# Performance work log

Measured on AMD Instinct MI355X. Metric: run time of the kernel, lower is better.

The kernel has to match this reference:

```python
import jax, jax.numpy as jnp
import numpy as np

H, HS, C = 16, 64, 1024  # num_heads, head_size, n_embd

def setup_inputs() -> dict:
    key = jax.random.key(0)
    ks = jax.random.split(key, 5)
    B, T = 2, 2048
    s = 1.0 / np.sqrt(C)
    return {
        "x": jax.random.normal(ks[0], (B, T, C), dtype=jnp.float32),
        "Wq": jax.random.normal(ks[1], (H, C, HS), dtype=jnp.float32) * s,
        "Wk": jax.random.normal(ks[2], (H, C, HS), dtype=jnp.float32) * s,
        "Wv": jax.random.normal(ks[3], (H, C, HS), dtype=jnp.float32) * s,
        "Wo": jax.random.normal(ks[4], (C, C), dtype=jnp.float32) * s,
    }

def reference(x, Wq, Wk, Wv, Wo):
    B, T, Cdim = x.shape
    scale = Cdim ** -0.5  # original scales by n_embd**-0.5, not head_size
    q = jnp.einsum('btc,hcd->bhtd', x, Wq)
    k = jnp.einsum('btc,hcd->bhtd', x, Wk)
    v = jnp.einsum('btc,hcd->bhtd', x, Wv)
    wei = jnp.einsum('bhtd,bhsd->bhts', q, k) * scale  # [B,H,T,T]
    causal = jnp.tril(jnp.ones((T, T), dtype=bool))
    wei = jnp.where(causal, wei, -jnp.inf)
    wei = jax.nn.softmax(wei, axis=-1)
    out = jnp.einsum('bhts,bhsd->bhtd', wei, v)  # [B,H,T,HS]
    out = out.transpose(0, 2, 1, 3).reshape(B, T, -1)  # concat heads -> [B,T,C]
    return out @ Wo.T
```

## Files before the change

### kernel.cpp

```cpp
#include <hip/hip_runtime.h>

typedef unsigned short ushort_t;
typedef __bf16 bf16x8 __attribute__((ext_vector_type(8)));
typedef float f32x4 __attribute__((ext_vector_type(4)));
typedef float f32x16 __attribute__((ext_vector_type(16)));
typedef unsigned short ushortx8 __attribute__((ext_vector_type(8)));
typedef unsigned int uintx4 __attribute__((ext_vector_type(4)));

#define NH 16
#define HS 64
#define CD 1024
#define NB 2
#define NT 2048
#define BT (NB * NT)
#define N3 (3 * CD)

#define L2E_DIV32 0.04508422002778011f

#define QKV_LD 2048
#define SLOT_BYTES 18432
#define WAVE_BYTES 4608
#define R0_SLOTS 796

__constant__ static const int QB_TAB[32] = {
  10,10,15,15, 4, 9, 9,13,14,14,14,15, 8, 8,12,12,
  13,13, 3, 7, 7,11,11,11,12, 6, 6, 2, 5, 5, 1, 0};
__constant__ static const int T0_TAB[32] = {
   0,11, 0,11, 0, 0,10, 0, 0,10,20,22, 0, 9, 0, 9,
  10,19, 0, 0, 8, 0, 8,16,18, 0, 7, 0, 0, 6, 0, 0};
__constant__ static const int T1_TAB[32] = {
  11,22,11,22,10,10,20,10,10,20,30,32, 9,18, 9,18,
  19,28, 8, 8,16, 8,16,24,26, 7,14, 6, 6,12, 4, 2};
__constant__ static const int K_TAB[32] = {
   2, 2, 3, 3, 1, 2, 2, 3, 3, 3, 3, 3, 2, 2, 3, 3,
   3, 3, 1, 2, 2, 3, 3, 3, 3, 2, 2, 1, 2, 2, 1, 1};
__constant__ static const int MC_TAB[11][3] = {
  {28,29, 0}, {25,26, 0}, {19,20, 0}, {12,13, 0}, { 5, 6, 0}, { 0, 1, 0},
  {21,22,23}, {14,15,24}, { 7,16,17}, { 8, 9,10}, { 2, 3,11}};


__device__ __forceinline__ ushort_t bf16_rne(float f) {
  union { float f; unsigned u; } v; v.f = f;
  unsigned u = v.u;
  unsigned r = (u + 0x7FFFu + ((u >> 16) & 1u)) >> 16;
  return (ushort_t)r;
}

__device__ __forceinline__ float bf2f(ushort_t u) {
  union { unsigned u; float f; } v; v.u = ((unsigned)u) << 16; return v.f;
}

__device__ __forceinline__ void gload_lds16(const ushort_t* g, ushort_t* l) {
  __builtin_amdgcn_global_load_lds(
      (const __attribute__((address_space(1))) unsigned int*)g,
      (__attribute__((address_space(3))) unsigned int*)l, 16, 0, 0);
}

__device__ __forceinline__ f32x4 mfma16(ushortx8 a, ushortx8 b, f32x4 c) {
  return __builtin_amdgcn_mfma_f32_16x16x32_bf16(
      __builtin_bit_cast(bf16x8, a), __builtin_bit_cast(bf16x8, b), c, 0, 0, 0);
}

__device__ __forceinline__ f32x16 mfma32(ushortx8 a, ushortx8 b, f32x16 c) {
  return __builtin_amdgcn_mfma_f32_32x32x16_bf16(
      __builtin_bit_cast(bf16x8, a), __builtin_bit_cast(bf16x8, b), c, 0, 0, 0);
}

__device__ __forceinline__ unsigned cvt_pk_bf16(float lo, float hi) {
  unsigned r;
  asm("v_cvt_pk_bf16_f32 %0, %1, %2" : "=v"(r) : "v"(lo), "v"(hi));
  return r;
}

__device__ __forceinline__ void plswap(unsigned &a, unsigned &b) {
  asm volatile("v_permlane32_swap_b32 %0, %1" : "+v"(a), "+v"(b));
}

__device__ __forceinline__ const char* slot_ptr(const char* wsb, const char* dout, int s) {
  return (s < R0_SLOTS) ? wsb + (size_t)s * SLOT_BYTES
                        : dout + (size_t)(s - R0_SLOTS) * SLOT_BYTES;
}


__global__ __launch_bounds__(256)
void pack_cast2(const float4* __restrict__ x, ushort_t* __restrict__ xout,
                const float4* __restrict__ wo, ushort_t* __restrict__ woout) {
  const int bid = blockIdx.x;
  const float4* in = (bid < 4096) ? x : wo;
  ushort_t* out = (bid < 4096) ? xout : woout;
  const int i = ((bid < 4096) ? bid : (bid - 4096)) * 256 + threadIdx.x;
  const float4 v = in[i];
  ushort4 r;
  r.x = bf16_rne(v.x); r.y = bf16_rne(v.y);
  r.z = bf16_rne(v.z); r.w = bf16_rne(v.w);
  *(ushort4*)(out + (size_t)i * 4) = r;
}

__global__ __launch_bounds__(256)
void pack_wqkv(const float* __restrict__ Wq, const float* __restrict__ Wk,
               const float* __restrict__ Wv, ushort_t* __restrict__ out) {
  __shared__ ushort_t tile[64 * 66];
  const int sh = blockIdx.y;
  const int s = sh >> 4, h = sh & 15;
  const float* W = (s == 0) ? Wq : ((s == 1) ? Wk : Wv);
  const int c0 = blockIdx.x * 64;
  const int t = threadIdx.x;
#pragma unroll
  for (int j = 0; j < 16; ++j) {
    const int idx = t + j * 256;
    const int ci = idx >> 6, d = idx & 63;
    const float v = W[(size_t)(h * 1024 + c0 + ci) * 64 + d];
    tile[d * 66 + ci] = bf16_rne(v);
  }
  __syncthreads();
#pragma unroll
  for (int j = 0; j < 16; ++j) {
    const int idx = t + j * 256;
    const int d = idx >> 6, ci = idx & 63;
    out[(size_t)(s * 1024 + h * 64 + d) * 1024 + c0 + ci] = tile[d * 66 + ci];
  }
}


template <int MODE>
__global__ __launch_bounds__(256)
void gemm_bt(const ushort_t* __restrict__ A, const ushort_t* __restrict__ Bt,
             void* __restrict__ Cv, ushort_t* __restrict__ Vt,
             int M, int N, int K) {
  __shared__ __align__(16) ushort_t ldsA[2][128 * 32];
  __shared__ __align__(16) ushort_t ldsB[2][128 * 32];
  const int tid = threadIdx.x;
  const int lane = tid & 63;
  const int wave = tid >> 6;
  const int row0 = blockIdx.y * 128;
  const int col0 = blockIdx.x * 128;
  const int wm = wave >> 1, wn = wave & 1;

  f32x4 acc[4][4] = {};

  const int ce = (tid & 3) * 8;

  auto stage = [&](int buf, int kt) {
    const int kbase = kt * 32;
#pragma unroll
    for (int j = 0; j < 2; ++j) {
      const int r = j * 64 + (tid >> 2);
      gload_lds16(A + (size_t)(row0 + r) * K + kbase + ce,
                  &ldsA[buf][(j * 256 + wave * 64) * 8]);
      gload_lds16(Bt + (size_t)(col0 + r) * K + kbase + ce,
                  &ldsB[buf][(j * 256 + wave * 64) * 8]);
    }
  };

  const int arow_off = (wm * 64 + (lane & 15)) * 32 + (lane >> 4) * 8;
  const int brow_off = (wn * 64 + (lane & 15)) * 32 + (lane >> 4) * 8;

  auto compute = [&](int buf) {
    ushortx8 af[4], bfr[4];
#pragma unroll
    for (int m = 0; m < 4; ++m)
      af[m] = *(const ushortx8*)&ldsA[buf][arow_off + m * 512];
#pragma unroll
    for (int n = 0; n < 4; ++n)
      bfr[n] = *(const ushortx8*)&ldsB[buf][brow_off + n * 512];
#pragma unroll
    for (int m = 0; m < 4; ++m)
#pragma unroll
      for (int n = 0; n < 4; ++n)
        acc[m][n] = mfma16(af[m], bfr[n], acc[m][n]);
  };

  stage(0, 0);
  __syncthreads();
  const int nk = K >> 5;
  for (int kt = 0; kt < nk; ++kt) {
    const int cur = kt & 1;
    if (kt + 1 < nk) stage(cur ^ 1, kt + 1);
    compute(cur);
    __syncthreads();
  }

#pragma unroll
  for (int m = 0; m < 4; ++m) {
    const int rbase = row0 + wm * 64 + m * 16 + (lane >> 4) * 4;
#pragma unroll
    for (int n = 0; n < 4; ++n) {
      const int col = col0 + wn * 64 + n * 16 + (lane & 15);
      if constexpr (MODE == 0) {
#pragma unroll
        for (int i = 0; i < 4; ++i)
          ((float*)Cv)[(size_t)(rbase + i) * N + col] = acc[m][n][i];
      } else {
        if (col < 2048) {
          const float sc = (col < 1024) ? L2E_DIV32 : 1.0f;
#pragma unroll
          for (int i = 0; i < 4; ++i)
            ((ushort_t*)Cv)[(size_t)(rbase + i) * QKV_LD + col] =
                bf16_rne(acc[m][n][i] * sc);
        } else {
          const int dcol = col - 2048;
          const int bI = rbase >> 11;
          const int t0i = rbase & 2047;
          ushort4 pk;
          pk.x = bf16_rne(acc[m][n][0]);
          pk.y = bf16_rne(acc[m][n][1]);
          pk.z = bf16_rne(acc[m][n][2]);
          pk.w = bf16_rne(acc[m][n][3]);
          *(ushort4*)(Vt + (size_t)(bI * 1024 + dcol) * NT + t0i) = pk;
        }
      }
    }
  }
}


__global__ __launch_bounds__(256, 4)
void attn_fwd11(const ushort_t* __restrict__ QKV, const ushort_t* __restrict__ Vt,
                ushort_t* __restrict__ O, char* __restrict__ wsb,
                char* __restrict__ dout) {
  __shared__ __align__(16) ushort_t KV[2][2][4096];

  const int tid = threadIdx.x;
  const int lane = tid & 63;
  const int w = tid >> 6;
  const int l31 = lane & 31;
  const int h = lane >> 5;

  const int x = blockIdx.x;
  const int bh = x & 31;
  const int c = x >> 5;
  const int qb = QB_TAB[c];
  const int k  = K_TAB[c];
  const int t0 = T0_TAB[c];
  const int t1 = T1_TAB[c];
  const int nt = 2 * qb + 2;
  const bool lastc = (t1 == nt);

  const int b = bh >> 4, head = bh & 15;
  const size_t base = (size_t)b * NT * QKV_LD;
  const int qg = qb * 128 + w * 32 + l31;
  const int tmax = lastc ? (2 * qb + (w >> 1)) : (t1 - 1);

  int koff[4];
#pragma unroll
  for (int kc = 0; kc < 4; ++kc)
    koff[kc] = l31 * 128 + (((2 * kc + h) ^ (l31 & 7)) * 16);

  const int rowA = tid >> 3, ccA = tid & 7;
  const int rowB = 32 + rowA;
  const ushort_t* kg = QKV + base + 1024 + head * 64;
  const ushort_t* vg = Vt + (size_t)(bh * 64) * NT;
  const ushort_t* ksA = kg + (size_t)(t0 * 64 + rowA) * QKV_LD + ((ccA ^ (rowA & 7)) * 8);
  const ushort_t* ksB = kg + (size_t)(t0 * 64 + rowB) * QKV_LD + ((ccA ^ (rowB & 7)) * 8);
  const ushort_t* vsA = vg + (size_t)rowA * NT + t0 * 64 + ((ccA ^ (rowA & 7)) * 8);
  const ushort_t* vsB = vg + (size_t)rowB * NT + t0 * 64 + ((ccA ^ (rowB & 7)) * 8);
  const size_t kadv = (size_t)64 * QKV_LD;

  gload_lds16(ksA, &KV[0][0][w * 512]);
  gload_lds16(ksB, &KV[0][0][2048 + w * 512]);
  gload_lds16(vsA, &KV[0][1][w * 512]);
  gload_lds16(vsB, &KV[0][1][2048 + w * 512]);

  ushortx8 qf[4];
  {
    const ushort_t* qp = QKV + base + (size_t)qg * QKV_LD + head * 64 + h * 8;
#pragma unroll
    for (int kc = 0; kc < 4; ++kc) qf[kc] = *(const ushortx8*)(qp + kc * 16);
  }

  f32x16 oA = {}, oB = {};
  float m_r = -INFINITY, l_r = 0.f;

  auto half_pass = [&](f32x16 s, const char* vb, const int kc0, const bool msk) {
    if (msk) {
#pragma unroll
      for (int r = 0; r < 16; ++r) {
        const int krow = (r & 3) + 8 * (r >> 2) + 4 * h;
        if (krow > l31) s[r] = -INFINITY;
      }
    }
    float mm[8];
#pragma unroll
    for (int r = 0; r < 8; ++r) mm[r] = fmaxf(s[r], s[r + 8]);
#pragma unroll
    for (int st = 4; st >= 1; st >>= 1)
#pragma unroll
      for (int r = 0; r < st; ++r) mm[r] = fmaxf(mm[r], mm[r + st]);
    const float mx = fmaxf(mm[0], __shfl_xor(mm[0], 32, 64));
    if (__any(mx > m_r + 8.0f)) {
      const float mn = fmaxf(m_r, mx);
      const float al = exp2f(m_r - mn);
      m_r = mn; l_r *= al;
#pragma unroll
      for (int r = 0; r < 16; ++r) { oA[r] *= al; oB[r] *= al; }
    }
    unsigned u[8];
    float ps[4];
#pragma unroll
    for (int jj = 0; jj < 4; ++jj) ps[jj] = 0.f;
#pragma unroll
    for (int jj = 0; jj < 8; ++jj) {
      const float e0 = exp2f(s[2 * jj] - m_r);
      const float e1 = exp2f(s[2 * jj + 1] - m_r);
      u[jj] = cvt_pk_bf16(e0, e1);
      ps[jj & 3] += e0 + e1;
    }
    ps[0] += ps[2]; ps[1] += ps[3]; ps[0] += ps[1];
    l_r += ps[0] + __shfl_xor(ps[0], 32, 64);
    plswap(u[0], u[2]); plswap(u[1], u[3]);
    plswap(u[4], u[6]); plswap(u[5], u[7]);
#pragma unroll
    for (int q2 = 0; q2 < 2; ++q2) {
      uintx4 pw;
      pw[0] = u[4 * q2 + 0]; pw[1] = u[4 * q2 + 1];
      pw[2] = u[4 * q2 + 2]; pw[3] = u[4 * q2 + 3];
      const ushortx8 pav = __builtin_bit_cast(ushortx8, pw);
      oA = mfma32(*(const ushortx8*)(vb + koff[kc0 + q2]), pav, oA);
      oB = mfma32(*(const ushortx8*)(vb + 4096 + koff[kc0 + q2]), pav, oB);
    }
  };

  int curb = 0;
  for (int t = t0; t < t1; ++t) {
    const int nxt = curb ^ 1;
    if (t + 1 < t1) {
      ksA += kadv; ksB += kadv; vsA += 64; vsB += 64;
      gload_lds16(ksA, &KV[nxt][0][w * 512]);
      gload_lds16(ksB, &KV[nxt][0][2048 + w * 512]);
      gload_lds16(vsA, &KV[nxt][1][w * 512]);
      gload_lds16(vsB, &KV[nxt][1][2048 + w * 512]);
      asm volatile("s_waitcnt vmcnt(4)" ::: "memory");
    } else {
      asm volatile("s_waitcnt vmcnt(0)" ::: "memory");
    }
    __builtin_amdgcn_s_barrier();
    asm volatile("" ::: "memory");

    if (t <= tmax) {
      const bool diag = lastc && (t == tmax);
      const bool halfB = diag && ((w & 1) == 0);
      const char* kb = (const char*)&KV[curb][0][0];
      const char* vb = (const char*)&KV[curb][1][0];

      {
        f32x16 sA = {};
#pragma unroll
        for (int kc = 0; kc < 4; ++kc)
          sA = mfma32(*(const ushortx8*)(kb + koff[kc]), qf[kc], sA);
        half_pass(sA, vb, 0, diag && halfB);
      }
      if (!halfB) {
        f32x16 sB = {};
#pragma unroll
        for (int kc = 0; kc < 4; ++kc)
          sB = mfma32(*(const ushortx8*)(kb + 4096 + koff[kc]), qf[kc], sB);
        half_pass(sB, vb, 2, diag);
      }
    }

    __builtin_amdgcn_s_barrier();
    asm volatile("" ::: "memory");
    curb ^= 1;
  }

  if (k == 1) {
    const float inv_l = 1.0f / l_r;
    ushort_t* op = O + ((size_t)(b * NT + qg)) * 1024 + head * 64;
#pragma unroll
    for (int db = 0; db < 2; ++db)
#pragma unroll
      for (int g = 0; g < 4; ++g) {
        ushort4 pk;
        pk.x = bf16_rne((db ? oB[4 * g + 0] : oA[4 * g + 0]) * inv_l);
        pk.y = bf16_rne((db ? oB[4 * g + 1] : oA[4 * g + 1]) * inv_l);
        pk.z = bf16_rne((db ? oB[4 * g + 2] : oA[4 * g + 2]) * inv_l);
        pk.w = bf16_rne((db ? oB[4 * g + 3] : oA[4 * g + 3]) * inv_l);
        *(ushort4*)(op + db * 32 + 8 * g + 4 * h) = pk;
      }
  } else {
    const int s = bh * 32 + c;
    char* wb = (char*)slot_ptr(wsb, dout, s) + w * WAVE_BYTES;
#pragma unroll
    for (int g = 0; g < 4; ++g) {
      ushortx8 pk;
#pragma unroll
      for (int e2 = 0; e2 < 8; ++e2)
        pk[e2] = bf16_rne(g < 2 ? oA[g * 8 + e2] : oB[(g - 2) * 8 + e2]);
      *(ushortx8*)(wb + lane * 64 + g * 16) = pk;
    }
    *(float*)(wb + 4096 + lane * 4) = m_r;
    *(float*)(wb + 4352 + lane * 4) = l_r;
  }
}

__global__ __launch_bounds__(256)
void attn_merge(const char* __restrict__ wsb, const char* __restrict__ dout,
                ushort_t* __restrict__ O) {
  const int x = blockIdx.x;
  const int bh = x & 31;
  const int qi = x >> 5;
  const int qb = 5 + qi;
  const int k = (qb <= 10) ? 2 : 3;
  const int tid = threadIdx.x;
  const int lane = tid & 63;
  const int w = tid >> 6;
  const int l31 = lane & 31;
  const int h = lane >> 5;

  float M = -INFINITY;
  for (int jj = 0; jj < k; ++jj) {
    const int s = bh * 32 + MC_TAB[qi][jj];
    const char* wb = slot_ptr(wsb, dout, s) + w * WAVE_BYTES;
    M = fmaxf(M, *(const float*)(wb + 4096 + lane * 4));
  }
  float o[32];
#pragma unroll
  for (int r = 0; r < 32; ++r) o[r] = 0.f;
  float lacc = 0.f;
  for (int jj = 0; jj < k; ++jj) {
    const int s = bh * 32 + MC_TAB[qi][jj];
    const char* wb = slot_ptr(wsb, dout, s) + w * WAVE_BYTES;
    const float a = exp2f(*(const float*)(wb + 4096 + lane * 4) - M);
    lacc += a * *(const float*)(wb + 4352 + lane * 4);
#pragma unroll
    for (int g = 0; g < 4; ++g) {
      const ushortx8 v = *(const ushortx8*)(wb + lane * 64 + g * 16);
#pragma unroll
      for (int e = 0; e < 8; ++e) o[g * 8 + e] += a * bf2f(v[e]);
    }
  }
  const float inv_l = 1.0f / lacc;
  const int b = bh >> 4, head = bh & 15;
  const int qg = qb * 128 + w * 32 + l31;
  ushort_t* op = O + ((size_t)(b * NT + qg)) * 1024 + head * 64;
#pragma unroll
  for (int db = 0; db < 2; ++db)
#pragma unroll
    for (int g = 0; g < 4; ++g) {
      ushort4 pk;
      pk.x = bf16_rne(o[db * 16 + 4 * g + 0] * inv_l);
      pk.y = bf16_rne(o[db * 16 + 4 * g + 1] * inv_l);
      pk.z = bf16_rne(o[db * 16 + 4 * g + 2] * inv_l);
      pk.w = bf16_rne(o[db * 16 + 4 * g + 3] * inv_l);
      *(ushort4*)(op + db * 32 + 8 * g + 4 * h) = pk;
    }
}


extern "C" void kernel_launch(void* const* d_in, const int* in_sizes, int n_in,
                              void* d_out, int out_size, void* d_ws, size_t ws_size,
                              hipStream_t stream) {
  (void)in_sizes; (void)n_in; (void)out_size; (void)ws_size;
  const float* x  = (const float*)d_in[0];
  const float* Wq = (const float*)d_in[1];
  const float* Wk = (const float*)d_in[2];
  const float* Wv = (const float*)d_in[3];
  const float* Wo = (const float*)d_in[4];

  char* ws = (char*)d_ws;
  ushort_t* Xbf    = (ushort_t*)(ws);
  ushort_t* Wqkv_t = (ushort_t*)(ws + 8388608);
  ushort_t* Wo_bf  = (ushort_t*)(ws + 14680064);
  ushort_t* QKV    = (ushort_t*)(ws + 16777216);
  ushort_t* Vt     = (ushort_t*)(ws + 33554432);
  ushort_t* Obf    = (ushort_t*)(ws + 41943040);

  pack_cast2<<<5120, 256, 0, stream>>>((const float4*)x, Xbf, (const float4*)Wo, Wo_bf);
  pack_wqkv<<<dim3(16, 48), 256, 0, stream>>>(Wq, Wk, Wv, Wqkv_t);

  gemm_bt<1><<<dim3(24, 32), 256, 0, stream>>>(Xbf, Wqkv_t, QKV, Vt, BT, N3, CD);
  attn_fwd11<<<1024, 256, 0, stream>>>(QKV, Vt, Obf, ws, (char*)d_out);
  attn_merge<<<352, 256, 0, stream>>>(ws, (char*)d_out, Obf);
  gemm_bt<0><<<dim3(8, 32), 256, 0, stream>>>(Obf, Wo_bf, d_out, nullptr, BT, CD, CD);
}
```

Baseline: 122.8 us.

## Split GEMM kernels, use 128x64 tiles for output projection, add MFMA priority hints

Splits the templated GEMM into a dedicated QKV kernel and a new 128x64-tile GEMM for the output projection. The new tile doubles the grid from 256 to 512 blocks so the CUs stay busier. The attention kernel now raises wave priority around its MFMA sequences with s_setprio and uses a flatter 3-way max tree for the row max. The smaller tile brings lower per-block reuse and more redundant A loads.

```diff
diff --git a/kernel.cpp b/kernel.cpp
--- a/kernel.cpp
+++ b/kernel.cpp
@@ -122,11 +122,9 @@
 }
 
 
-template <int MODE>
 __global__ __launch_bounds__(256)
-void gemm_bt(const ushort_t* __restrict__ A, const ushort_t* __restrict__ Bt,
-             void* __restrict__ Cv, ushort_t* __restrict__ Vt,
-             int M, int N, int K) {
+void gemm_bt_qkv(const ushort_t* __restrict__ A, const ushort_t* __restrict__ Bt,
+                 ushort_t* __restrict__ QKVo, ushort_t* __restrict__ Vt, int K) {
   __shared__ __align__(16) ushort_t ldsA[2][128 * 32];
   __shared__ __align__(16) ushort_t ldsB[2][128 * 32];
   const int tid = threadIdx.x;
@@ -186,36 +184,99 @@
 #pragma unroll
     for (int n = 0; n < 4; ++n) {
       const int col = col0 + wn * 64 + n * 16 + (lane & 15);
-      if constexpr (MODE == 0) {
+      if (col < 2048) {
+        const float sc = (col < 1024) ? L2E_DIV32 : 1.0f;
 #pragma unroll
         for (int i = 0; i < 4; ++i)
-          ((float*)Cv)[(size_t)(rbase + i) * N + col] = acc[m][n][i];
+          QKVo[(size_t)(rbase + i) * QKV_LD + col] = bf16_rne(acc[m][n][i] * sc);
       } else {
-        if (col < 2048) {
-          const float sc = (col < 1024) ? L2E_DIV32 : 1.0f;
-#pragma unroll
-          for (int i = 0; i < 4; ++i)
-            ((ushort_t*)Cv)[(size_t)(rbase + i) * QKV_LD + col] =
-                bf16_rne(acc[m][n][i] * sc);
-        } else {
-          const int dcol = col - 2048;
-          const int bI = rbase >> 11;
-          const int t0i = rbase & 2047;
-          ushort4 pk;
-          pk.x = bf16_rne(acc[m][n][0]);
-          pk.y = bf16_rne(acc[m][n][1]);
-          pk.z = bf16_rne(acc[m][n][2]);
-          pk.w = bf16_rne(acc[m][n][3]);
-          *(ushort4*)(Vt + (size_t)(bI * 1024 + dcol) * NT + t0i) = pk;
-        }
+        const int dcol = col - 2048;
+        const int bI = rbase >> 11;
+        const int t0i = rbase & 2047;
+        ushort4 pk;
+        pk.x = bf16_rne(acc[m][n][0]);
+        pk.y = bf16_rne(acc[m][n][1]);
+        pk.z = bf16_rne(acc[m][n][2]);
+        pk.w = bf16_rne(acc[m][n][3]);
+        *(ushort4*)(Vt + (size_t)(bI * 1024 + dcol) * NT + t0i) = pk;
       }
     }
   }
 }
 
 
+__global__ __launch_bounds__(256)
+void gemm_bt64(const ushort_t* __restrict__ A, const ushort_t* __restrict__ Bt,
+               float* __restrict__ C, int M, int N, int K) {
+  __shared__ __align__(16) ushort_t ldsA[2][128 * 32];
+  __shared__ __align__(16) ushort_t ldsB[2][64 * 32];
+  const int tid = threadIdx.x;
+  const int lane = tid & 63;
+  const int wave = tid >> 6;
+  const int row0 = blockIdx.y * 128;
+  const int col0 = blockIdx.x * 64;
+  const int wm = wave >> 1, wn = wave & 1;
+
+  f32x4 acc[4][2] = {};
+
+  const int ce = (tid & 3) * 8;
+
+  auto stage = [&](int buf, int kt) {
+    const int kbase = kt * 32;
+#pragma unroll
+    for (int j = 0; j < 2; ++j) {
+      const int r = j * 64 + (tid >> 2);
+      gload_lds16(A + (size_t)(row0 + r) * K + kbase + ce,
+                  &ldsA[buf][(j * 256 + wave * 64) * 8]);
+    }
+    gload_lds16(Bt + (size_t)(col0 + (tid >> 2)) * K + kbase + ce,
+                &ldsB[buf][(wave * 64) * 8]);
+  };
+
+  const int arow_off = (wm * 64 + (lane & 15)) * 32 + (lane >> 4) * 8;
+  const int brow_off = (wn * 32 + (lane & 15)) * 32 + (lane >> 4) * 8;
+
+  auto compute = [&](int buf) {
+    ushortx8 af[4], bfr[2];
+#pragma unroll
+    for (int m = 0; m < 4; ++m)
+      af[m] = *(const ushortx8*)&ldsA[buf][arow_off + m * 512];
+#pragma unroll
+    for (int n = 0; n < 2; ++n)
+      bfr[n] = *(const ushortx8*)&ldsB[buf][brow_off + n * 512];
+#pragma unroll
+    for (int m = 0; m < 4; ++m)
+#pragma unroll
+      for (int n = 0; n < 2; ++n)
+        acc[m][n] = mfma16(af[m], bfr[n], acc[m][n]);
+  };
+
+  stage(0, 0);
+  __syncthreads();
+  const int nk = K >> 5;
+  for (int kt = 0; kt < nk; ++kt) {
+    const int cur = kt & 1;
+    if (kt + 1 < nk) stage(cur ^ 1, kt + 1);
+    compute(cur);
+    __syncthreads();
+  }
+
+#pragma unroll
+  for (int m = 0; m < 4; ++m) {
+    const int rbase = row0 + wm * 64 + m * 16 + (lane >> 4) * 4;
+#pragma unroll
+    for (int n = 0; n < 2; ++n) {
+      const int col = col0 + wn * 32 + n * 16 + (lane & 15);
+#pragma unroll
+      for (int i = 0; i < 4; ++i)
+        C[(size_t)(rbase + i) * N + col] = acc[m][n][i];
+    }
+  }
+}
+
+
 __global__ __launch_bounds__(256, 4)
-void attn_fwd11(const ushort_t* __restrict__ QKV, const ushort_t* __restrict__ Vt,
+void attn_fwd13(const ushort_t* __restrict__ QKV, const ushort_t* __restrict__ Vt,
                 ushort_t* __restrict__ O, char* __restrict__ wsb,
                 char* __restrict__ dout) {
   __shared__ __align__(16) ushort_t KV[2][2][4096];
@@ -279,14 +340,15 @@
         if (krow > l31) s[r] = -INFINITY;
       }
     }
-    float mm[8];
-#pragma unroll
-    for (int r = 0; r < 8; ++r) mm[r] = fmaxf(s[r], s[r + 8]);
-#pragma unroll
-    for (int st = 4; st >= 1; st >>= 1)
-#pragma unroll
-      for (int r = 0; r < st; ++r) mm[r] = fmaxf(mm[r], mm[r + st]);
-    const float mx = fmaxf(mm[0], __shfl_xor(mm[0], 32, 64));
+    const float t0m = fmaxf(fmaxf(s[0], s[1]), s[2]);
+    const float t1m = fmaxf(fmaxf(s[3], s[4]), s[5]);
+    const float t2m = fmaxf(fmaxf(s[6], s[7]), s[8]);
+    const float t3m = fmaxf(fmaxf(s[9], s[10]), s[11]);
+    const float t4m = fmaxf(fmaxf(s[12], s[13]), s[14]);
+    const float u0m = fmaxf(fmaxf(t0m, t1m), t2m);
+    const float u1m = fmaxf(fmaxf(t3m, t4m), s[15]);
+    float mx = fmaxf(u0m, u1m);
+    mx = fmaxf(mx, __shfl_xor(mx, 32, 64));
     if (__any(mx > m_r + 8.0f)) {
       const float mn = fmaxf(m_r, mx);
       const float al = exp2f(m_r - mn);
@@ -309,6 +371,7 @@
     l_r += ps[0] + __shfl_xor(ps[0], 32, 64);
     plswap(u[0], u[2]); plswap(u[1], u[3]);
     plswap(u[4], u[6]); plswap(u[5], u[7]);
+    __builtin_amdgcn_s_setprio(1);
 #pragma unroll
     for (int q2 = 0; q2 < 2; ++q2) {
       uintx4 pw;
@@ -318,6 +381,7 @@
       oA = mfma32(*(const ushortx8*)(vb + koff[kc0 + q2]), pav, oA);
       oB = mfma32(*(const ushortx8*)(vb + 4096 + koff[kc0 + q2]), pav, oB);
     }
+    __builtin_amdgcn_s_setprio(0);
   };
 
   int curb = 0;
@@ -344,16 +408,20 @@
 
       {
         f32x16 sA = {};
+        __builtin_amdgcn_s_setprio(1);
 #pragma unroll
         for (int kc = 0; kc < 4; ++kc)
           sA = mfma32(*(const ushortx8*)(kb + koff[kc]), qf[kc], sA);
+        __builtin_amdgcn_s_setprio(0);
         half_pass(sA, vb, 0, diag && halfB);
       }
       if (!halfB) {
         f32x16 sB = {};
+        __builtin_amdgcn_s_setprio(1);
 #pragma unroll
         for (int kc = 0; kc < 4; ++kc)
           sB = mfma32(*(const ushortx8*)(kb + 4096 + koff[kc]), qf[kc], sB);
+        __builtin_amdgcn_s_setprio(0);
         half_pass(sB, vb, 2, diag);
       }
     }
@@ -468,8 +536,8 @@
   pack_cast2<<<5120, 256, 0, stream>>>((const float4*)x, Xbf, (const float4*)Wo, Wo_bf);
   pack_wqkv<<<dim3(16, 48), 256, 0, stream>>>(Wq, Wk, Wv, Wqkv_t);
 
-  gemm_bt<1><<<dim3(24, 32), 256, 0, stream>>>(Xbf, Wqkv_t, QKV, Vt, BT, N3, CD);
-  attn_fwd11<<<1024, 256, 0, stream>>>(QKV, Vt, Obf, ws, (char*)d_out);
+  gemm_bt_qkv<<<dim3(24, 32), 256, 0, stream>>>(Xbf, Wqkv_t, QKV, Vt, CD);
+  attn_fwd13<<<1024, 256, 0, stream>>>(QKV, Vt, Obf, ws, (char*)d_out);
   attn_merge<<<352, 256, 0, stream>>>(ws, (char*)d_out, Obf);
-  gemm_bt<0><<<dim3(8, 32), 256, 0, stream>>>(Obf, Wo_bf, d_out, nullptr, BT, CD, CD);
-}
+  gemm_bt64<<<dim3(16, 32), 256, 0, stream>>>(Obf, Wo_bf, (float*)d_out, BT, CD, CD);
+}
```

Result: faster. 119.5 us (-2.7%).
